# Kernel tuning notes

Measured on AMD Instinct MI355X. Metric: run time of the kernel, lower is better.

Reference implementation:

```python
import jax, jax.numpy as jnp
import numpy as np
import math

B, S, DIM = 2, 2048, 1024
H, D = 16, 64  # num_head, head_dim; H*D == DIM

def setup_inputs() -> dict:
    key = jax.random.key(0)
    ks = jax.random.split(key, 10)
    s = 0.02
    return {
        "X": jax.random.normal(ks[0], (B, S, DIM), dtype=jnp.float32),
        "mask": jnp.ones((B, S), dtype=jnp.float32),
        "Wq": jax.random.normal(ks[1], (DIM, H * D), dtype=jnp.float32) * s,
        "bq": jnp.zeros((H * D,), dtype=jnp.float32),
        "Wk": jax.random.normal(ks[2], (DIM, H * D), dtype=jnp.float32) * s,
        "bk": jnp.zeros((H * D,), dtype=jnp.float32),
        "Wv": jax.random.normal(ks[3], (DIM, H * D), dtype=jnp.float32) * s,
        "bv": jnp.zeros((H * D,), dtype=jnp.float32),
        "Wo": jax.random.normal(ks[4], (H * D, DIM), dtype=jnp.float32) * s,
        "bo": jnp.zeros((DIM,), dtype=jnp.float32),
    }

def _split_heads(x):
    # [B, S, H*D] -> [B, H, S, D]
    b, s, _ = x.shape
    return x.reshape(b, s, H, D).transpose(0, 2, 1, 3)

def reference(X, mask, Wq, bq, Wk, bk, Wv, bv, Wo, bo):
    Q = _split_heads(X @ Wq + bq)
    K = _split_heads(X @ Wk + bk)
    V = _split_heads(X @ Wv + bv)
    # scaled dot-product attention with additive mask penalty
    dot = jnp.einsum('bhqd,bhkd->bhqk', Q, K) / math.sqrt(D)
    dot = dot - 1e6 * (1.0 - mask[:, None, None, :])
    attn = jax.nn.softmax(dot, axis=-1)
    ctx = jnp.einsum('bhqk,bhkd->bhqd', attn, V)
    # combine heads: [B, H, S, D] -> [B, S, H*D]
    ctx = ctx.transpose(0, 2, 1, 3).reshape(B, S, H * D)
    return ctx @ Wo + bo
```

## Files before the change

kernel.cpp:

```cpp
#include <hip/hip_runtime.h>
#include <cstdint>
#include <cstddef>

typedef __attribute__((ext_vector_type(8))) _Float16 f16x8;
typedef __attribute__((ext_vector_type(4))) _Float16 f16x4;
typedef __attribute__((ext_vector_type(4))) float f32x4;

#define MFMA_16x16x32(a, b, c) __builtin_amdgcn_mfma_f32_16x16x32_f16((a), (b), (c), 0, 0, 0)

static constexpr int kB = 2, kS = 2048, kDim = 1024, kH = 16, kD = 64;
static constexpr int kM = kB * kS;
static constexpr float kQScale = 0.125f * 1.44269504088896340736f;

__global__ void cvt_f32_to_f16(const float* __restrict__ in, _Float16* __restrict__ out, int n8) {
  int i = blockIdx.x * blockDim.x + threadIdx.x;
  if (i >= n8) return;
  const float4* p = (const float4*)in + (size_t)i * 2;
  float4 a = p[0], b = p[1];
  f16x8 h;
  h[0] = (_Float16)a.x; h[1] = (_Float16)a.y; h[2] = (_Float16)a.z; h[3] = (_Float16)a.w;
  h[4] = (_Float16)b.x; h[5] = (_Float16)b.y; h[6] = (_Float16)b.z; h[7] = (_Float16)b.w;
  ((f16x8*)out)[i] = h;
}

__global__ void transpose_cvt_w(const float* __restrict__ w0, const float* __restrict__ w1,
                                const float* __restrict__ w2, const float* __restrict__ w3,
                                _Float16* __restrict__ o0, _Float16* __restrict__ o1,
                                _Float16* __restrict__ o2, _Float16* __restrict__ o3) {
  const float* w; _Float16* o;
  switch (blockIdx.z) {
    case 0: w = w0; o = o0; break;
    case 1: w = w1; o = o1; break;
    case 2: w = w2; o = o2; break;
    default: w = w3; o = o3; break;
  }
  __shared__ alignas(16) _Float16 tile[64][72];
  const int kt = blockIdx.x * 64;
  const int nt = blockIdx.y * 64;
  const int tr = threadIdx.x >> 4;
  const int tc = threadIdx.x & 15;
#pragma unroll
  for (int rr = 0; rr < 4; ++rr) {
    int r = rr * 16 + tr;
    float4 v = *(const float4*)&w[(size_t)(kt + r) * kDim + nt + tc * 4];
    f16x4 hv;
    hv[0] = (_Float16)v.x; hv[1] = (_Float16)v.y; hv[2] = (_Float16)v.z; hv[3] = (_Float16)v.w;
    *(f16x4*)&tile[r][tc * 4] = hv;
  }
  __syncthreads();
#pragma unroll
  for (int rr = 0; rr < 4; ++rr) {
    int nl = rr * 16 + tr;
    f16x4 hv;
    hv[0] = tile[tc * 4 + 0][nl];
    hv[1] = tile[tc * 4 + 1][nl];
    hv[2] = tile[tc * 4 + 2][nl];
    hv[3] = tile[tc * 4 + 3][nl];
    *(f16x4*)&o[(size_t)(nt + nl) * kDim + kt + tc * 4] = hv;
  }
}

__global__ void mask_penalty(const float* __restrict__ mask, float* __restrict__ pen, int n) {
  int i = blockIdx.x * blockDim.x + threadIdx.x;
  if (i < n) pen[i] = -1.0e6f * (1.0f - mask[i]) * 1.44269504088896340736f;
}

__global__ __launch_bounds__(256, 2) void gemm_qkv(
    const _Float16* __restrict__ A,
    const _Float16* __restrict__ wt0, const _Float16* __restrict__ wt1, const _Float16* __restrict__ wt2,
    const float* __restrict__ bias0, const float* __restrict__ bias1, const float* __restrict__ bias2,
    _Float16* __restrict__ oq, _Float16* __restrict__ ok, _Float16* __restrict__ ov) {
  const _Float16* Bt; const float* bias; _Float16* out;
  switch (blockIdx.z) {
    case 0: Bt = wt0; bias = bias0; out = oq; break;
    case 1: Bt = wt1; bias = bias1; out = ok; break;
    default: Bt = wt2; bias = bias2; out = ov; break;
  }
  const bool isV = (blockIdx.z == 2);
  __shared__ alignas(16) _Float16 As[2][128 * 72];
  __shared__ alignas(16) _Float16 Bs[2][128 * 72];
  const int tid = threadIdx.x;
  const int lane = tid & 63;
  const int wave = tid >> 6;
  const int wm = wave & 1, wn = wave >> 1;
  const int l15 = lane & 15, quad = lane >> 4;
  const int m0 = blockIdx.x * 128, n0 = blockIdx.y * 128;

  const int srow = tid >> 3;
  const int skc = (tid & 7) * 8;

  f32x4 acc[4][4] = {};
  f16x8 ra[4], rb[4];

#pragma unroll
  for (int i = 0; i < 4; ++i) {
    int row = srow + 32 * i;
    ra[i] = *(const f16x8*)&A[(size_t)(m0 + row) * kDim + skc];
    rb[i] = *(const f16x8*)&Bt[(size_t)(n0 + row) * kDim + skc];
  }
#pragma unroll
  for (int i = 0; i < 4; ++i) {
    int row = srow + 32 * i;
    *(f16x8*)&As[0][row * 72 + skc] = ra[i];
    *(f16x8*)&Bs[0][row * 72 + skc] = rb[i];
  }

  for (int kt = 0; kt < 16; ++kt) {
    const int cur = kt & 1;
    if (kt + 1 < 16) {
      int k0 = (kt + 1) * 64;
#pragma unroll
      for (int i = 0; i < 4; ++i) {
        int row = srow + 32 * i;
        ra[i] = *(const f16x8*)&A[(size_t)(m0 + row) * kDim + k0 + skc];
        rb[i] = *(const f16x8*)&Bt[(size_t)(n0 + row) * kDim + k0 + skc];
      }
    }
    __syncthreads();
#pragma unroll
    for (int kk = 0; kk < 2; ++kk) {
      f16x8 af[4], bf[4];
#pragma unroll
      for (int t = 0; t < 4; ++t) af[t] = *(const f16x8*)&As[cur][(wm * 64 + t * 16 + l15) * 72 + kk * 32 + quad * 8];
#pragma unroll
      for (int t = 0; t < 4; ++t) bf[t] = *(const f16x8*)&Bs[cur][(wn * 64 + t * 16 + l15) * 72 + kk * 32 + quad * 8];
      if (isV) {
#pragma unroll
        for (int i = 0; i < 4; ++i)
#pragma unroll
          for (int j = 0; j < 4; ++j)
            acc[i][j] = MFMA_16x16x32(af[i], bf[j], acc[i][j]);
      } else {
#pragma unroll
        for (int i = 0; i < 4; ++i)
#pragma unroll
          for (int j = 0; j < 4; ++j)
            acc[i][j] = MFMA_16x16x32(bf[i], af[j], acc[i][j]);
      }
    }
    if (kt + 1 < 16) {
#pragma unroll
      for (int i = 0; i < 4; ++i) {
        int row = srow + 32 * i;
        *(f16x8*)&As[cur ^ 1][row * 72 + skc] = ra[i];
        *(f16x8*)&Bs[cur ^ 1][row * 72 + skc] = rb[i];
      }
    }
  }

  if (isV) {
    const int mbase = m0 + wm * 64 + quad * 4;
    const int nbase = n0 + wn * 64 + l15;
#pragma unroll
    for (int j = 0; j < 4; ++j) {
      int n = nbase + j * 16;
      float bv = bias[n];
      int h = n >> 6, d = n & 63;
#pragma unroll
      for (int i = 0; i < 4; ++i) {
        int m = mbase + i * 16;
        int b = m >> 11, s = m & (kS - 1);
        f16x4 hv;
#pragma unroll
        for (int r = 0; r < 4; ++r) hv[r] = (_Float16)(acc[i][j][r] + bv);
        *(f16x4*)&out[((size_t)((b * kH + h) * kD + d)) * kS + s] = hv;
      }
    }
  } else {
    const float osc = (blockIdx.z == 0) ? kQScale : 1.0f;
#pragma unroll
    for (int i = 0; i < 4; ++i) {
      int nb = n0 + wn * 64 + i * 16 + quad * 4;
      f32x4 bv4 = *(const f32x4*)&bias[nb];
      int hh = nb >> 6, d0 = nb & 63;
#pragma unroll
      for (int j = 0; j < 4; ++j) {
        int m = m0 + wm * 64 + j * 16 + l15;
        int bb = m >> 11, s = m & (kS - 1);
        f16x4 hv;
#pragma unroll
        for (int r = 0; r < 4; ++r) hv[r] = (_Float16)((acc[i][j][r] + bv4[r]) * osc);
        *(f16x4*)&out[((size_t)((bb * kH + hh) * kS) + s) * kD + d0] = hv;
      }
    }
  }
}

__global__ __launch_bounds__(256, 2) void attn(
    const _Float16* __restrict__ Q, const _Float16* __restrict__ K,
    const _Float16* __restrict__ V, const float* __restrict__ pen2,
    _Float16* __restrict__ ctx) {
  const int bh = blockIdx.y;
  const int b = bh >> 4;
  const int q0 = blockIdx.x * 128;
  const int tid = threadIdx.x, lane = tid & 63, wave = tid >> 6;
  const int l15 = lane & 15, quad = lane >> 4;

  __shared__ alignas(16) _Float16 Ks[128 * 72];
  __shared__ alignas(16) _Float16 Vs[64 * 136];
  __shared__ alignas(16) _Float16 Pt[4][16 * 136];
  __shared__ alignas(16) float pens[128];

  const _Float16* Qh = Q + (size_t)bh * kS * kD;
  const _Float16* Kh = K + (size_t)bh * kS * kD;
  const _Float16* Vh = V + (size_t)bh * kS * kD;

  f16x8 qf[2][2];
#pragma unroll
  for (int t = 0; t < 2; ++t) {
    int qrow = q0 + wave * 32 + t * 16 + l15;
#pragma unroll
    for (int kk = 0; kk < 2; ++kk)
      qf[t][kk] = *(const f16x8*)&Qh[(size_t)qrow * kD + kk * 32 + quad * 8];
  }

  f32x4 o_acc[2][4] = {};
  float l_part[2] = {0.0f, 0.0f};

  for (int kb = 0; kb < kS; kb += 128) {
    __syncthreads();
#pragma unroll
    for (int i = 0; i < 4; ++i) {
      int c = tid + 256 * i;
      int row = c >> 3, dc = (c & 7) * 8;
      *(f16x8*)&Ks[row * 72 + dc] = *(const f16x8*)&Kh[(size_t)(kb + row) * kD + dc];
    }
#pragma unroll
    for (int i = 0; i < 4; ++i) {
      int c = tid + 256 * i;
      int row = c >> 4, sc8 = (c & 15) * 8;
      *(f16x8*)&Vs[row * 136 + sc8] = *(const f16x8*)&Vh[(size_t)row * kS + kb + sc8];
    }
    if (tid < 128) pens[tid] = pen2[b * kS + kb + tid];
    __syncthreads();

    f32x4 s[2][8] = {};
#pragma unroll
    for (int kk = 0; kk < 2; ++kk)
#pragma unroll
      for (int colt = 0; colt < 8; ++colt) {
        f16x8 kf = *(const f16x8*)&Ks[(colt * 16 + l15) * 72 + kk * 32 + quad * 8];
        s[0][colt] = MFMA_16x16x32(kf, qf[0][kk], s[0][colt]);
        s[1][colt] = MFMA_16x16x32(kf, qf[1][kk], s[1][colt]);
      }

#pragma unroll
    for (int t = 0; t < 2; ++t) {
#pragma unroll
      for (int colt = 0; colt < 8; ++colt) {
        f32x4 pn = *(const f32x4*)&pens[colt * 16 + quad * 4];
        f16x4 ph;
#pragma unroll
        for (int r = 0; r < 4; ++r) {
          float pv = __builtin_exp2f(s[t][colt][r] + pn[r]);
          l_part[t] += pv;
          ph[r] = (_Float16)pv;
        }
        *(f16x4*)&Pt[wave][l15 * 136 + colt * 16 + quad * 4] = ph;
      }
#pragma unroll
      for (int ks = 0; ks < 4; ++ks) {
        f16x8 pf = *(const f16x8*)&Pt[wave][l15 * 136 + ks * 32 + quad * 8];
#pragma unroll
        for (int c = 0; c < 4; ++c) {
          f16x8 vf = *(const f16x8*)&Vs[(c * 16 + l15) * 136 + ks * 32 + quad * 8];
          o_acc[t][c] = MFMA_16x16x32(vf, pf, o_acc[t][c]);
        }
      }
    }
  }

  const int h = bh & 15;
#pragma unroll
  for (int t = 0; t < 2; ++t) {
    float lsum = l_part[t];
    lsum += __shfl_xor(lsum, 16, 64);
    lsum += __shfl_xor(lsum, 32, 64);
    float inv = 1.0f / lsum;
    int q = q0 + wave * 32 + t * 16 + l15;
#pragma unroll
    for (int c = 0; c < 4; ++c) {
      f16x4 oh;
#pragma unroll
      for (int r = 0; r < 4; ++r) oh[r] = (_Float16)(o_acc[t][c][r] * inv);
      *(f16x4*)&ctx[((size_t)(b * kS + q)) * kDim + h * kD + c * 16 + quad * 4] = oh;
    }
  }
}

__global__ __launch_bounds__(256, 2) void gemm_out(
    const _Float16* __restrict__ A, const _Float16* __restrict__ Bt,
    const float* __restrict__ bias, float* __restrict__ out) {
  __shared__ alignas(16) _Float16 As[2][128 * 72];
  __shared__ alignas(16) _Float16 Bs[2][128 * 72];
  const int tid = threadIdx.x;
  const int lane = tid & 63;
  const int wave = tid >> 6;
  const int wm = wave & 1, wn = wave >> 1;
  const int l15 = lane & 15, quad = lane >> 4;
  const int m0 = blockIdx.x * 128, n0 = blockIdx.y * 128;

  const int srow = tid >> 3;
  const int skc = (tid & 7) * 8;

  f32x4 acc[4][4] = {};
  f16x8 ra[4], rb[4];

#pragma unroll
  for (int i = 0; i < 4; ++i) {
    int row = srow + 32 * i;
    ra[i] = *(const f16x8*)&A[(size_t)(m0 + row) * kDim + skc];
    rb[i] = *(const f16x8*)&Bt[(size_t)(n0 + row) * kDim + skc];
  }
#pragma unroll
  for (int i = 0; i < 4; ++i) {
    int row = srow + 32 * i;
    *(f16x8*)&As[0][row * 72 + skc] = ra[i];
    *(f16x8*)&Bs[0][row * 72 + skc] = rb[i];
  }

  for (int kt = 0; kt < 16; ++kt) {
    const int cur = kt & 1;
    if (kt + 1 < 16) {
      int k0 = (kt + 1) * 64;
#pragma unroll
      for (int i = 0; i < 4; ++i) {
        int row = srow + 32 * i;
        ra[i] = *(const f16x8*)&A[(size_t)(m0 + row) * kDim + k0 + skc];
        rb[i] = *(const f16x8*)&Bt[(size_t)(n0 + row) * kDim + k0 + skc];
      }
    }
    __syncthreads();
#pragma unroll
    for (int kk = 0; kk < 2; ++kk) {
      f16x8 af[4], bf[4];
#pragma unroll
      for (int t = 0; t < 4; ++t) af[t] = *(const f16x8*)&As[cur][(wm * 64 + t * 16 + l15) * 72 + kk * 32 + quad * 8];
#pragma unroll
      for (int t = 0; t < 4; ++t) bf[t] = *(const f16x8*)&Bs[cur][(wn * 64 + t * 16 + l15) * 72 + kk * 32 + quad * 8];
#pragma unroll
      for (int i = 0; i < 4; ++i)
#pragma unroll
        for (int j = 0; j < 4; ++j)
          acc[i][j] = MFMA_16x16x32(bf[i], af[j], acc[i][j]);
    }
    if (kt + 1 < 16) {
#pragma unroll
      for (int i = 0; i < 4; ++i) {
        int row = srow + 32 * i;
        *(f16x8*)&As[cur ^ 1][row * 72 + skc] = ra[i];
        *(f16x8*)&Bs[cur ^ 1][row * 72 + skc] = rb[i];
      }
    }
  }

#pragma unroll
  for (int i = 0; i < 4; ++i) {
    int nb = n0 + wn * 64 + i * 16 + quad * 4;
    f32x4 bv4 = *(const f32x4*)&bias[nb];
#pragma unroll
    for (int j = 0; j < 4; ++j) {
      int m = m0 + wm * 64 + j * 16 + l15;
      f32x4 ov;
#pragma unroll
      for (int r = 0; r < 4; ++r) ov[r] = acc[i][j][r] + bv4[r];
      *(f32x4*)&out[(size_t)m * kDim + nb] = ov;
    }
  }
}

extern "C" void kernel_launch(void* const* d_in, const int* in_sizes, int n_in,
                              void* d_out, int out_size, void* d_ws, size_t ws_size,
                              hipStream_t stream) {
  (void)in_sizes; (void)n_in; (void)out_size; (void)ws_size;
  const float* X    = (const float*)d_in[0];
  const float* mask = (const float*)d_in[1];
  const float* Wq   = (const float*)d_in[2];
  const float* bq   = (const float*)d_in[3];
  const float* Wk   = (const float*)d_in[4];
  const float* bk   = (const float*)d_in[5];
  const float* Wv   = (const float*)d_in[6];
  const float* bv   = (const float*)d_in[7];
  const float* Wo   = (const float*)d_in[8];
  const float* bo   = (const float*)d_in[9];
  float* out = (float*)d_out;

  char* ws = (char*)d_ws;
  _Float16* Xh   = (_Float16*)(ws);
  _Float16* Wqt  = (_Float16*)(ws + ((size_t)8  << 20));
  _Float16* Wkt  = (_Float16*)(ws + ((size_t)10 << 20));
  _Float16* Wvt  = (_Float16*)(ws + ((size_t)12 << 20));
  _Float16* Wot  = (_Float16*)(ws + ((size_t)14 << 20));
  _Float16* Qh   = (_Float16*)(ws + ((size_t)16 << 20));
  _Float16* Kh   = (_Float16*)(ws + ((size_t)24 << 20));
  _Float16* Vh   = (_Float16*)(ws + ((size_t)32 << 20));
  _Float16* Ch   = (_Float16*)(ws + ((size_t)40 << 20));
  float*    pen2 = (float*)   (ws + ((size_t)48 << 20));

  cvt_f32_to_f16<<<dim3(kM * kDim / 8 / 256), dim3(256), 0, stream>>>(X, Xh, kM * kDim / 8);
  transpose_cvt_w<<<dim3(16, 16, 4), dim3(256), 0, stream>>>(Wq, Wk, Wv, Wo, Wqt, Wkt, Wvt, Wot);
  mask_penalty<<<dim3(16), dim3(256), 0, stream>>>(mask, pen2, kB * kS);
  gemm_qkv<<<dim3(32, 8, 3), dim3(256), 0, stream>>>(Xh, Wqt, Wkt, Wvt, bq, bk, bv, Qh, Kh, Vh);
  attn<<<dim3(16, 32), dim3(256), 0, stream>>>(Qh, Kh, Vh, pen2, Ch);
  gemm_out<<<dim3(32, 8), dim3(256), 0, stream>>>(Ch, Wot, bo, out);
}
```

Before: 228.5 us.

## Fuse Q/K/V projections into one GEMM sharing A tile; batch PV MFMAs

The QKV projection becomes a single kernel in which each block loads one 128-row X tile and three 64-column weight tiles, computing Q, K and V together. This reuses the A tile three times instead of once per z-slice. The register-prefetch double buffering is dropped in favour of a simple load-sync-compute loop, which may expose global memory latency. In attention, P is now written for both 16-row query tiles first, so each V fragment load feeds two MFMAs, at the cost of twice the P scratch in shared memory.

```diff
diff --git a/kernel.cpp b/kernel.cpp
--- a/kernel.cpp
+++ b/kernel.cpp
@@ -65,123 +65,104 @@
   if (i < n) pen[i] = -1.0e6f * (1.0f - mask[i]) * 1.44269504088896340736f;
 }
 
-__global__ __launch_bounds__(256, 2) void gemm_qkv(
+__global__ __launch_bounds__(256, 2) void gemm_qkv3(
     const _Float16* __restrict__ A,
-    const _Float16* __restrict__ wt0, const _Float16* __restrict__ wt1, const _Float16* __restrict__ wt2,
-    const float* __restrict__ bias0, const float* __restrict__ bias1, const float* __restrict__ bias2,
+    const _Float16* __restrict__ wtq, const _Float16* __restrict__ wtk, const _Float16* __restrict__ wtv,
+    const float* __restrict__ bq, const float* __restrict__ bk, const float* __restrict__ bv,
     _Float16* __restrict__ oq, _Float16* __restrict__ ok, _Float16* __restrict__ ov) {
-  const _Float16* Bt; const float* bias; _Float16* out;
-  switch (blockIdx.z) {
-    case 0: Bt = wt0; bias = bias0; out = oq; break;
-    case 1: Bt = wt1; bias = bias1; out = ok; break;
-    default: Bt = wt2; bias = bias2; out = ov; break;
-  }
-  const bool isV = (blockIdx.z == 2);
-  __shared__ alignas(16) _Float16 As[2][128 * 72];
-  __shared__ alignas(16) _Float16 Bs[2][128 * 72];
+  __shared__ alignas(16) _Float16 As[128 * 72];
+  __shared__ alignas(16) _Float16 Bqs[64 * 72];
+  __shared__ alignas(16) _Float16 Bks[64 * 72];
+  __shared__ alignas(16) _Float16 Bvs[64 * 72];
   const int tid = threadIdx.x;
   const int lane = tid & 63;
   const int wave = tid >> 6;
   const int wm = wave & 1, wn = wave >> 1;
   const int l15 = lane & 15, quad = lane >> 4;
-  const int m0 = blockIdx.x * 128, n0 = blockIdx.y * 128;
-
-  const int srow = tid >> 3;
-  const int skc = (tid & 7) * 8;
-
-  f32x4 acc[4][4] = {};
-  f16x8 ra[4], rb[4];
-
-#pragma unroll
-  for (int i = 0; i < 4; ++i) {
-    int row = srow + 32 * i;
-    ra[i] = *(const f16x8*)&A[(size_t)(m0 + row) * kDim + skc];
-    rb[i] = *(const f16x8*)&Bt[(size_t)(n0 + row) * kDim + skc];
-  }
-#pragma unroll
-  for (int i = 0; i < 4; ++i) {
-    int row = srow + 32 * i;
-    *(f16x8*)&As[0][row * 72 + skc] = ra[i];
-    *(f16x8*)&Bs[0][row * 72 + skc] = rb[i];
-  }
-
-  for (int kt = 0; kt < 16; ++kt) {
-    const int cur = kt & 1;
-    if (kt + 1 < 16) {
-      int k0 = (kt + 1) * 64;
-#pragma unroll
-      for (int i = 0; i < 4; ++i) {
-        int row = srow + 32 * i;
-        ra[i] = *(const f16x8*)&A[(size_t)(m0 + row) * kDim + k0 + skc];
-        rb[i] = *(const f16x8*)&Bt[(size_t)(n0 + row) * kDim + k0 + skc];
-      }
+  const int m0 = blockIdx.x * 128, n0 = blockIdx.y * 64;
+
+  f32x4 acc_q[2][4] = {};
+  f32x4 acc_k[2][4] = {};
+  f32x4 acc_v[4][2] = {};
+
+  for (int k0 = 0; k0 < kDim; k0 += 64) {
+    __syncthreads();
+#pragma unroll
+    for (int i = 0; i < 4; ++i) {
+      int c = tid + 256 * i;
+      int row = c >> 3, kc = (c & 7) * 8;
+      *(f16x8*)&As[row * 72 + kc] = *(const f16x8*)&A[(size_t)(m0 + row) * kDim + k0 + kc];
+    }
+#pragma unroll
+    for (int i = 0; i < 2; ++i) {
+      int c = tid + 256 * i;
+      int row = c >> 3, kc = (c & 7) * 8;
+      *(f16x8*)&Bqs[row * 72 + kc] = *(const f16x8*)&wtq[(size_t)(n0 + row) * kDim + k0 + kc];
+      *(f16x8*)&Bks[row * 72 + kc] = *(const f16x8*)&wtk[(size_t)(n0 + row) * kDim + k0 + kc];
+      *(f16x8*)&Bvs[row * 72 + kc] = *(const f16x8*)&wtv[(size_t)(n0 + row) * kDim + k0 + kc];
     }
     __syncthreads();
 #pragma unroll
     for (int kk = 0; kk < 2; ++kk) {
-      f16x8 af[4], bf[4];
-#pragma unroll
-      for (int t = 0; t < 4; ++t) af[t] = *(const f16x8*)&As[cur][(wm * 64 + t * 16 + l15) * 72 + kk * 32 + quad * 8];
-#pragma unroll
-      for (int t = 0; t < 4; ++t) bf[t] = *(const f16x8*)&Bs[cur][(wn * 64 + t * 16 + l15) * 72 + kk * 32 + quad * 8];
-      if (isV) {
-#pragma unroll
-        for (int i = 0; i < 4; ++i)
-#pragma unroll
-          for (int j = 0; j < 4; ++j)
-            acc[i][j] = MFMA_16x16x32(af[i], bf[j], acc[i][j]);
-      } else {
-#pragma unroll
-        for (int i = 0; i < 4; ++i)
-#pragma unroll
-          for (int j = 0; j < 4; ++j)
-            acc[i][j] = MFMA_16x16x32(bf[i], af[j], acc[i][j]);
-      }
-    }
-    if (kt + 1 < 16) {
-#pragma unroll
-      for (int i = 0; i < 4; ++i) {
-        int row = srow + 32 * i;
-        *(f16x8*)&As[cur ^ 1][row * 72 + skc] = ra[i];
-        *(f16x8*)&Bs[cur ^ 1][row * 72 + skc] = rb[i];
-      }
-    }
-  }
-
-  if (isV) {
-    const int mbase = m0 + wm * 64 + quad * 4;
-    const int nbase = n0 + wn * 64 + l15;
+      f16x8 af[4], bqf[2], bkf[2], bvf[2];
+#pragma unroll
+      for (int t = 0; t < 4; ++t) af[t] = *(const f16x8*)&As[(wm * 64 + t * 16 + l15) * 72 + kk * 32 + quad * 8];
+#pragma unroll
+      for (int t = 0; t < 2; ++t) {
+        int brow = (wn * 32 + t * 16 + l15) * 72 + kk * 32 + quad * 8;
+        bqf[t] = *(const f16x8*)&Bqs[brow];
+        bkf[t] = *(const f16x8*)&Bks[brow];
+        bvf[t] = *(const f16x8*)&Bvs[brow];
+      }
+#pragma unroll
+      for (int i = 0; i < 2; ++i)
+#pragma unroll
+        for (int j = 0; j < 4; ++j) {
+          acc_q[i][j] = MFMA_16x16x32(bqf[i], af[j], acc_q[i][j]);
+          acc_k[i][j] = MFMA_16x16x32(bkf[i], af[j], acc_k[i][j]);
+        }
+#pragma unroll
+      for (int j = 0; j < 4; ++j)
+#pragma unroll
+        for (int i = 0; i < 2; ++i)
+          acc_v[j][i] = MFMA_16x16x32(af[j], bvf[i], acc_v[j][i]);
+    }
+  }
+
+#pragma unroll
+  for (int i = 0; i < 2; ++i) {
+    int nb = n0 + wn * 32 + i * 16 + quad * 4;
+    f32x4 bq4 = *(const f32x4*)&bq[nb];
+    f32x4 bk4 = *(const f32x4*)&bk[nb];
+    int hh = nb >> 6, d0 = nb & 63;
 #pragma unroll
     for (int j = 0; j < 4; ++j) {
-      int n = nbase + j * 16;
-      float bv = bias[n];
-      int h = n >> 6, d = n & 63;
-#pragma unroll
-      for (int i = 0; i < 4; ++i) {
-        int m = mbase + i * 16;
-        int b = m >> 11, s = m & (kS - 1);
-        f16x4 hv;
-#pragma unroll
-        for (int r = 0; r < 4; ++r) hv[r] = (_Float16)(acc[i][j][r] + bv);
-        *(f16x4*)&out[((size_t)((b * kH + h) * kD + d)) * kS + s] = hv;
-      }
-    }
-  } else {
-    const float osc = (blockIdx.z == 0) ? kQScale : 1.0f;
-#pragma unroll
-    for (int i = 0; i < 4; ++i) {
-      int nb = n0 + wn * 64 + i * 16 + quad * 4;
-      f32x4 bv4 = *(const f32x4*)&bias[nb];
-      int hh = nb >> 6, d0 = nb & 63;
-#pragma unroll
-      for (int j = 0; j < 4; ++j) {
-        int m = m0 + wm * 64 + j * 16 + l15;
-        int bb = m >> 11, s = m & (kS - 1);
-        f16x4 hv;
-#pragma unroll
-        for (int r = 0; r < 4; ++r) hv[r] = (_Float16)((acc[i][j][r] + bv4[r]) * osc);
-        *(f16x4*)&out[((size_t)((bb * kH + hh) * kS) + s) * kD + d0] = hv;
-      }
+      int m = m0 + wm * 64 + j * 16 + l15;
+      int bb = m >> 11, s = m & (kS - 1);
+      size_t base = ((size_t)((bb * kH + hh) * kS) + s) * kD + d0;
+      f16x4 hq, hk;
+#pragma unroll
+      for (int r = 0; r < 4; ++r) {
+        hq[r] = (_Float16)((acc_q[i][j][r] + bq4[r]) * kQScale);
+        hk[r] = (_Float16)(acc_k[i][j][r] + bk4[r]);
+      }
+      *(f16x4*)&oq[base] = hq;
+      *(f16x4*)&ok[base] = hk;
+    }
+  }
+#pragma unroll
+  for (int i = 0; i < 2; ++i) {
+    int n = n0 + wn * 32 + i * 16 + l15;
+    float bvv = bv[n];
+    int hh = n >> 6, d = n & 63;
+#pragma unroll
+    for (int j = 0; j < 4; ++j) {
+      int m = m0 + wm * 64 + j * 16 + quad * 4;
+      int bb = m >> 11, s = m & (kS - 1);
+      f16x4 hv;
+#pragma unroll
+      for (int r = 0; r < 4; ++r) hv[r] = (_Float16)(acc_v[j][i][r] + bvv);
+      *(f16x4*)&ov[((size_t)((bb * kH + hh) * kD + d)) * kS + s] = hv;
     }
   }
 }
@@ -198,7 +179,7 @@
 
   __shared__ alignas(16) _Float16 Ks[128 * 72];
   __shared__ alignas(16) _Float16 Vs[64 * 136];
-  __shared__ alignas(16) _Float16 Pt[4][16 * 136];
+  __shared__ alignas(16) _Float16 Pt[4][32 * 136];
   __shared__ alignas(16) float pens[128];
 
   const _Float16* Qh = Q + (size_t)bh * kS * kD;
@@ -256,16 +237,19 @@
           l_part[t] += pv;
           ph[r] = (_Float16)pv;
         }
-        *(f16x4*)&Pt[wave][l15 * 136 + colt * 16 + quad * 4] = ph;
-      }
-#pragma unroll
-      for (int ks = 0; ks < 4; ++ks) {
-        f16x8 pf = *(const f16x8*)&Pt[wave][l15 * 136 + ks * 32 + quad * 8];
-#pragma unroll
-        for (int c = 0; c < 4; ++c) {
-          f16x8 vf = *(const f16x8*)&Vs[(c * 16 + l15) * 136 + ks * 32 + quad * 8];
-          o_acc[t][c] = MFMA_16x16x32(vf, pf, o_acc[t][c]);
-        }
+        *(f16x4*)&Pt[wave][(t * 16 + l15) * 136 + colt * 16 + quad * 4] = ph;
+      }
+    }
+
+#pragma unroll
+    for (int ks = 0; ks < 4; ++ks) {
+      f16x8 pf0 = *(const f16x8*)&Pt[wave][(l15) * 136 + ks * 32 + quad * 8];
+      f16x8 pf1 = *(const f16x8*)&Pt[wave][(16 + l15) * 136 + ks * 32 + quad * 8];
+#pragma unroll
+      for (int c = 0; c < 4; ++c) {
+        f16x8 vf = *(const f16x8*)&Vs[(c * 16 + l15) * 136 + ks * 32 + quad * 8];
+        o_acc[0][c] = MFMA_16x16x32(vf, pf0, o_acc[0][c]);
+        o_acc[1][c] = MFMA_16x16x32(vf, pf1, o_acc[1][c]);
       }
     }
   }
@@ -400,7 +384,7 @@
   cvt_f32_to_f16<<<dim3(kM * kDim / 8 / 256), dim3(256), 0, stream>>>(X, Xh, kM * kDim / 8);
   transpose_cvt_w<<<dim3(16, 16, 4), dim3(256), 0, stream>>>(Wq, Wk, Wv, Wo, Wqt, Wkt, Wvt, Wot);
   mask_penalty<<<dim3(16), dim3(256), 0, stream>>>(mask, pen2, kB * kS);
-  gemm_qkv<<<dim3(32, 8, 3), dim3(256), 0, stream>>>(Xh, Wqt, Wkt, Wvt, bq, bk, bv, Qh, Kh, Vh);
+  gemm_qkv3<<<dim3(32, 16), dim3(256), 0, stream>>>(Xh, Wqt, Wkt, Wvt, bq, bk, bv, Qh, Kh, Vh);
   attn<<<dim3(16, 32), dim3(256), 0, stream>>>(Qh, Kh, Vh, pen2, Ch);
   gemm_out<<<dim3(32, 8), dim3(256), 0, stream>>>(Ch, Wot, bo, out);
 }
```

Result: faster. 221.3 us (-3.2%).
